# Kernel optimization log

Measured on AMD Instinct MI355X. Metric: run time of the kernel, lower is better.

The kernel has to match this reference:

```python
import jax, jax.numpy as jnp
import numpy as np

B, T, I, H = 512, 256, 256, 512


def _lstm(x, Wih, Whh, bih, bhh):
    # x: [B, T, I]; Wih: [4H, I]; Whh: [4H, H]; gate order i, f, g, o (torch)
    Bv = x.shape[0]
    Hv = Whh.shape[1]
    xg = jnp.einsum('bti,gi->btg', x, Wih) + bih + bhh  # [B, T, 4H] (input projections hoisted out of scan)
    xg = jnp.transpose(xg, (1, 0, 2))  # [T, B, 4H]
    h0 = jnp.zeros((Bv, Hv), x.dtype)
    c0 = jnp.zeros((Bv, Hv), x.dtype)

    def step(carry, gx):
        h, c = carry
        g = gx + h @ Whh.T  # [B, 4H]
        i, f, gg, o = jnp.split(g, 4, axis=-1)
        i = jax.nn.sigmoid(i)
        f = jax.nn.sigmoid(f)
        gg = jnp.tanh(gg)
        o = jax.nn.sigmoid(o)
        c = f * c + i * gg
        h = o * jnp.tanh(c)
        return (h, c), h

    _, hs = jax.lax.scan(step, (h0, c0), xg)  # hs: [T, B, H]
    return jnp.transpose(hs, (1, 0, 2))  # [B, T, H]


def _bn1d(x, gamma, beta, eps=1e-5):
    # torch BatchNorm1d on [N, C, L] in training mode: per-channel stats over (N, L), biased var
    m = jnp.mean(x, axis=(0, 2), keepdims=True)
    v = jnp.var(x, axis=(0, 2), keepdims=True)
    return (x - m) * jax.lax.rsqrt(v + eps) * gamma[None, :, None] + beta[None, :, None]


def setup_inputs() -> dict:
    key = jax.random.key(0)
    ks = jax.random.split(key, 14)
    s = 1.0 / np.sqrt(H)
    return {
        'x': jax.random.normal(ks[0], (B, T, I), jnp.float32),
        'Wih': jax.random.uniform(ks[1], (4 * H, I), jnp.float32, -s, s),
        'Whh': jax.random.uniform(ks[2], (4 * H, H), jnp.float32, -s, s),
        'bih': jax.random.uniform(ks[3], (4 * H,), jnp.float32, -s, s),
        'bhh': jax.random.uniform(ks[4], (4 * H,), jnp.float32, -s, s),
        'fc1_w': jax.random.uniform(ks[5], (32, H), jnp.float32, -s, s),
        'fc1_b': jax.random.uniform(ks[6], (32,), jnp.float32, -s, s),
        'fc2_w': jax.random.uniform(ks[7], (1, 32), jnp.float32, -0.17, 0.17),
        'fc2_b': jax.random.uniform(ks[8], (1,), jnp.float32, -0.17, 0.17),
        'bn1_g': jnp.ones((T,), jnp.float32),
        'bn1_b': jnp.zeros((T,), jnp.float32),
        'bn2_g': jnp.ones((T,), jnp.float32),
        'bn2_b': jnp.zeros((T,), jnp.float32),
    }


def reference(x, Wih, Whh, bih, bhh, fc1_w, fc1_b, fc2_w, fc2_b, bn1_g, bn1_b, bn2_g, bn2_b):
    lstm_out = _lstm(x, Wih, Whh, bih, bhh)  # [B, T, H]
    a = jnp.einsum('bth,oh->bto', lstm_out, fc1_w) + fc1_b  # [B, T, 32]
    a = jax.nn.leaky_relu(_bn1d(a, bn1_g, bn1_b), negative_slope=0.1)
    z = jnp.einsum('bto,po->btp', a, fc2_w) + fc2_b  # [B, T, 1]
    out = jax.nn.relu(_bn1d(z, bn2_g, bn2_b))
    return out
```

## Files before the change

kernel.cpp:

```cpp
#include <hip/hip_runtime.h>

#define BB 512
#define TT 256
#define II 256
#define HH 512

typedef __attribute__((ext_vector_type(8))) short bf16x8;
typedef __attribute__((ext_vector_type(4))) float f32x4;

__device__ __forceinline__ unsigned short f2bf(float f) {
  union { float f; unsigned u; } v; v.f = f;
  unsigned r = v.u + 0x7fffu + ((v.u >> 16) & 1u);
  return (unsigned short)(r >> 16);
}

#define OFF_CNT   0
#define OFF_HSWZ  4096
#define OFF_XSWZ  1052672ULL
#define OFF_HIST  68161536ULL
#define ZERO_WORDS 263168

__global__ void zero_k(unsigned* __restrict__ p, int n) {
  int i = blockIdx.x * blockDim.x + threadIdx.x;
  if (i < n) p[i] = 0u;
}

__global__ __launch_bounds__(256) void prep_x(const float* __restrict__ x,
                                              unsigned char* __restrict__ ws) {
  __shared__ unsigned short xs[16][264];
  const int t = blockIdx.x >> 5, rc = blockIdx.x & 31;
  const int tid = threadIdx.x;
  {
    const int r = tid >> 4, seg = tid & 15;
    const float* src = x + ((size_t)(rc * 16 + r) * TT + t) * II + seg * 16;
    const float4* s4 = (const float4*)src;
#pragma unroll
    for (int q = 0; q < 4; ++q) {
      float4 v = s4[q];
      xs[r][seg * 16 + q * 4 + 0] = f2bf(v.x);
      xs[r][seg * 16 + q * 4 + 1] = f2bf(v.y);
      xs[r][seg * 16 + q * 4 + 2] = f2bf(v.z);
      xs[r][seg * 16 + q * 4 + 3] = f2bf(v.w);
    }
  }
  __syncthreads();
  const int lane = tid & 63;
  const int row16 = lane & 15, koff = (lane >> 4) * 8;
#pragma unroll
  for (int kc = tid >> 6; kc < 8; kc += 4) {
    union { unsigned short h[8]; uint4 v; } pk;
#pragma unroll
    for (int j = 0; j < 8; ++j) pk.h[j] = xs[row16][kc * 32 + koff + j];
    *(uint4*)(ws + OFF_XSWZ + (size_t)(t * 8 + kc) * 32768u +
              ((size_t)rc * 64 + lane) * 16) = pk.v;
  }
}

__global__ __launch_bounds__(512, 2) void lstm_persist(
    const float* __restrict__ Wih, const float* __restrict__ Whh,
    const float* __restrict__ bih, const float* __restrict__ bhh,
    unsigned char* __restrict__ ws)
{
  const int gid = blockIdx.x;
  const int group = gid & 7;
  const int m = gid >> 3;
  const int tid = threadIdx.x;
  const int wv = tid >> 6, lane = tid & 63;
  const int mb = wv & 3, kh = wv >> 2;
  const int lq = lane >> 4, ln = lane & 15;

  int* flags_g = (int*)(ws + OFF_CNT + (size_t)group * 512);
  unsigned char* xswz  = ws + OFF_XSWZ;
  unsigned char* hswz0 = ws + OFF_HSWZ;
  unsigned char* hswz1 = ws + OFF_HSWZ + 524288;
  unsigned char* hist  = ws + OFF_HIST;

  __shared__ int step_flag;
  if (tid == 0) step_flag = 0;

  bf16x8 Wf[12][4];
#pragma unroll
  for (int kk = 0; kk < 12; ++kk) {
    const int kb = (kh * 12 + kk) * 32 + lq * 8;
#pragma unroll
    for (int nt = 0; nt < 4; ++nt) {
      const int gcol = nt * 512 + m * 16 + ln;
      const float* s = (kb < 256) ? (Wih + (size_t)gcol * 256 + kb)
                                  : (Whh + (size_t)gcol * 512 + (kb - 256));
      bf16x8 w;
#pragma unroll
      for (int j = 0; j < 8; ++j) w[j] = (short)f2bf(s[j]);
      Wf[kk][nt] = w;
    }
  }

  float bia[4];
#pragma unroll
  for (int nt = 0; nt < 4; ++nt) {
    int gcol = nt * 512 + m * 16 + ln;
    bia[nt] = bih[gcol] + bhh[gcol];
  }

  __shared__ float g_s[64 * 68];
  __shared__ float h_s[64 * 17];

  const size_t aoff = ((size_t)(group * 4 + mb) * 64 + lane) * 16;
  float creg[4] = {0.f, 0.f, 0.f, 0.f};
  const f32x4 zero4 = {0.f, 0.f, 0.f, 0.f};

#pragma unroll 1
  for (int t = 0; t < 256; ++t) {
    unsigned char* hrd = (t & 1) ? hswz1 : hswz0;
    unsigned char* hwr = (t & 1) ? hswz0 : hswz1;

    f32x4 acc[4] = {zero4, zero4, zero4, zero4};

    if (kh == 0) {
#pragma unroll
      for (int kk = 0; kk < 8; ++kk) {
        bf16x8 a = *(const bf16x8*)(xswz + (size_t)(t * 8 + kk) * 32768u + aoff);
#pragma unroll
        for (int nt = 0; nt < 4; ++nt)
          acc[nt] = __builtin_amdgcn_mfma_f32_16x16x32_bf16(a, Wf[kk][nt], acc[nt], 0, 0, 0);
      }
    }

    if (t > 0) {
      if (kh == 1) {
        int iter = 0;
        for (;;) {
          int v = __hip_atomic_load(flags_g + (lane & 31),
                                    __ATOMIC_RELAXED, __HIP_MEMORY_SCOPE_AGENT);
          if (__all(v >= t)) break;
          if (++iter >= (1 << 17)) break;
          __builtin_amdgcn_s_sleep(1);
        }
        if (wv == 4)
          __hip_atomic_store(&step_flag, t, __ATOMIC_RELAXED,
                             __HIP_MEMORY_SCOPE_WORKGROUP);
      } else {
        int iter = 0;
        while (__hip_atomic_load(&step_flag, __ATOMIC_RELAXED,
                                 __HIP_MEMORY_SCOPE_WORKGROUP) < t
               && iter < (1 << 20)) {
          ++iter;
          __builtin_amdgcn_s_sleep(1);
        }
      }
    }

    if (kh == 0) {
      unsigned long long u0[4], u1[4];
#pragma unroll
      for (int p = 0; p < 4; ++p) {
        const unsigned long long* q =
            (const unsigned long long*)(hrd + (size_t)p * 32768u + aoff);
        u0[p] = __hip_atomic_load(q + 0, __ATOMIC_RELAXED, __HIP_MEMORY_SCOPE_AGENT);
        u1[p] = __hip_atomic_load(q + 1, __ATOMIC_RELAXED, __HIP_MEMORY_SCOPE_AGENT);
      }
#pragma unroll
      for (int kk = 0; kk < 4; ++kk) {
        union { unsigned long long q[2]; bf16x8 v; } u;
        u.q[0] = u0[kk]; u.q[1] = u1[kk];
#pragma unroll
        for (int nt = 0; nt < 4; ++nt)
          acc[nt] = __builtin_amdgcn_mfma_f32_16x16x32_bf16(u.v, Wf[8 + kk][nt], acc[nt], 0, 0, 0);
      }
    } else {
      unsigned long long u0[6], u1[6];
#pragma unroll
      for (int p = 0; p < 6; ++p) {
        const unsigned long long* q =
            (const unsigned long long*)(hrd + (size_t)(4 + p) * 32768u + aoff);
        u0[p] = __hip_atomic_load(q + 0, __ATOMIC_RELAXED, __HIP_MEMORY_SCOPE_AGENT);
        u1[p] = __hip_atomic_load(q + 1, __ATOMIC_RELAXED, __HIP_MEMORY_SCOPE_AGENT);
      }
#pragma unroll
      for (int kk = 0; kk < 12; ++kk) {
        const int slot = kk % 6;
        union { unsigned long long q[2]; bf16x8 v; } u;
        u.q[0] = u0[slot]; u.q[1] = u1[slot];
        if (kk < 6) {
          const unsigned long long* q =
              (const unsigned long long*)(hrd + (size_t)(10 + kk) * 32768u + aoff);
          u0[slot] = __hip_atomic_load(q + 0, __ATOMIC_RELAXED, __HIP_MEMORY_SCOPE_AGENT);
          u1[slot] = __hip_atomic_load(q + 1, __ATOMIC_RELAXED, __HIP_MEMORY_SCOPE_AGENT);
        }
#pragma unroll
        for (int nt = 0; nt < 4; ++nt)
          acc[nt] = __builtin_amdgcn_mfma_f32_16x16x32_bf16(u.v, Wf[kk][nt], acc[nt], 0, 0, 0);
      }
#pragma unroll
      for (int nt = 0; nt < 4; ++nt)
#pragma unroll
        for (int r = 0; r < 4; ++r)
          g_s[(mb * 16 + lq * 4 + r) * 68 + nt * 16 + ln] = acc[nt][r];
    }
    __syncthreads();

    if (kh == 0) {
#pragma unroll
      for (int r = 0; r < 4; ++r) {
        const int rw = mb * 16 + lq * 4 + r;
        float gi = acc[0][r] + g_s[rw * 68 + ln]      + bia[0];
        float gf = acc[1][r] + g_s[rw * 68 + 16 + ln] + bia[1];
        float gg = acc[2][r] + g_s[rw * 68 + 32 + ln] + bia[2];
        float go = acc[3][r] + g_s[rw * 68 + 48 + ln] + bia[3];
        float iv = 1.f / (1.f + __expf(-gi));
        float fv = 1.f / (1.f + __expf(-gf));
        float gv = 1.f - 2.f / (__expf(2.f * gg) + 1.f);
        float ov = 1.f / (1.f + __expf(-go));
        float cv = fv * creg[r] + iv * gv;
        creg[r] = cv;
        h_s[rw * 17 + ln] = ov * (1.f - 2.f / (__expf(2.f * cv) + 1.f));
      }
    }
    __syncthreads();

    if (tid < 256) {
      int rc_l = tid >> 6;
      int rem = tid & 63;
      int lane_off = rem >> 1;
      int half = rem & 1;
      int l2 = (m & 1) * 32 + lane_off;
      int rowl = rc_l * 16 + (lane_off & 15);
      int jb = (lane_off >> 4) * 8 + half * 4;
      union { ushort4 s; unsigned long long q; } pk;
      pk.s = make_ushort4(f2bf(h_s[rowl * 17 + jb + 0]),
                          f2bf(h_s[rowl * 17 + jb + 1]),
                          f2bf(h_s[rowl * 17 + jb + 2]),
                          f2bf(h_s[rowl * 17 + jb + 3]));
      size_t off = ((size_t)((m >> 1) * 32 + group * 4 + rc_l) * 64 + l2) * 16 + half * 8;
      *(unsigned long long*)(hwr + off) = pk.q;
    }
    __syncthreads();

    if (tid == 0)
      __hip_atomic_store(flags_g + m, t + 1, __ATOMIC_RELAXED,
                         __HIP_MEMORY_SCOPE_AGENT);

    if (tid < 256) {
      int row = tid >> 2, jb = (tid & 3) * 4;
      ushort4 hq = make_ushort4(f2bf(h_s[row * 17 + jb + 0]),
                                f2bf(h_s[row * 17 + jb + 1]),
                                f2bf(h_s[row * 17 + jb + 2]),
                                f2bf(h_s[row * 17 + jb + 3]));
      int b = group * 64 + row;
      *(ushort4*)(hist + ((size_t)(b * 256 + t) * 512 + m * 16 + jb) * 2) = hq;
    }
  }
}

__global__ __launch_bounds__(256) void e1_fc1(
    const float* __restrict__ fc1_w, const unsigned char* __restrict__ hist,
    float* __restrict__ a_out)
{
  const int tid = threadIdx.x, wv = tid >> 6, lane = tid & 63;
  const int lq = lane >> 4, ln = lane & 15;

  bf16x8 Bf[16][2];
#pragma unroll
  for (int kk = 0; kk < 16; ++kk) {
#pragma unroll
    for (int nt = 0; nt < 2; ++nt) {
      const float* s = fc1_w + (size_t)(nt * 16 + ln) * 512 + kk * 32 + lq * 8;
      bf16x8 w;
#pragma unroll
      for (int j = 0; j < 8; ++j) w[j] = (short)f2bf(s[j]);
      Bf[kk][nt] = w;
    }
  }

  const int rbase = blockIdx.x * 128 + wv * 32;
  const f32x4 zero4 = {0.f, 0.f, 0.f, 0.f};
  f32x4 acc[2][2] = {{zero4, zero4}, {zero4, zero4}};
#pragma unroll
  for (int kk = 0; kk < 16; ++kk) {
    bf16x8 a0 = *(const bf16x8*)(hist + ((size_t)(rbase + ln) * 512 + kk * 32 + lq * 8) * 2);
    bf16x8 a1 = *(const bf16x8*)(hist + ((size_t)(rbase + 16 + ln) * 512 + kk * 32 + lq * 8) * 2);
#pragma unroll
    for (int nt = 0; nt < 2; ++nt) {
      acc[0][nt] = __builtin_amdgcn_mfma_f32_16x16x32_bf16(a0, Bf[kk][nt], acc[0][nt], 0, 0, 0);
      acc[1][nt] = __builtin_amdgcn_mfma_f32_16x16x32_bf16(a1, Bf[kk][nt], acc[1][nt], 0, 0, 0);
    }
  }
#pragma unroll
  for (int mt = 0; mt < 2; ++mt)
#pragma unroll
    for (int nt = 0; nt < 2; ++nt)
#pragma unroll
      for (int r = 0; r < 4; ++r) {
        int row = rbase + mt * 16 + lq * 4 + r;
        a_out[(size_t)row * 32 + nt * 16 + ln] = acc[mt][nt][r];
      }
}

__global__ __launch_bounds__(256) void e2_head(
    const float* __restrict__ a_in, const float* __restrict__ fc1_b,
    const float* __restrict__ fc2_w, const float* __restrict__ fc2_b,
    const float* __restrict__ bn1_g, const float* __restrict__ bn1_b,
    const float* __restrict__ bn2_g, const float* __restrict__ bn2_b,
    float* __restrict__ out)
{
  const int t = blockIdx.x, tid = threadIdx.x;
  __shared__ float fb[32], fw[32];
  __shared__ float red[4][2], red2[4][2];
  if (tid < 32) { fb[tid] = fc1_b[tid]; fw[tid] = fc2_w[tid]; }
  __syncthreads();

  float va[2][32];
  float s1 = 0.f, s2 = 0.f;
#pragma unroll
  for (int rr = 0; rr < 2; ++rr) {
    int b = tid * 2 + rr;
    const float* p = a_in + ((size_t)b * 256 + t) * 32;
#pragma unroll
    for (int o = 0; o < 32; ++o) {
      float v = p[o] + fb[o];
      va[rr][o] = v;
      s1 += v; s2 += v * v;
    }
  }
#pragma unroll
  for (int off = 32; off > 0; off >>= 1) {
    s1 += __shfl_down(s1, off);
    s2 += __shfl_down(s2, off);
  }
  if ((tid & 63) == 0) { red[tid >> 6][0] = s1; red[tid >> 6][1] = s2; }
  __syncthreads();
  float tot1 = red[0][0] + red[1][0] + red[2][0] + red[3][0];
  float tot2 = red[0][1] + red[1][1] + red[2][1] + red[3][1];
  float m1 = tot1 * (1.f / 16384.f);
  float v1 = tot2 * (1.f / 16384.f) - m1 * m1;
  float sc1 = bn1_g[t] * rsqrtf(v1 + 1e-5f);
  float sh1 = bn1_b[t];

  float z[2];
  float zs1 = 0.f, zs2 = 0.f;
#pragma unroll
  for (int rr = 0; rr < 2; ++rr) {
    float acc = fc2_b[0];
#pragma unroll
    for (int o = 0; o < 32; ++o) {
      float av = (va[rr][o] - m1) * sc1 + sh1;
      av = (av > 0.f) ? av : 0.1f * av;
      acc += av * fw[o];
    }
    z[rr] = acc; zs1 += acc; zs2 += acc * acc;
  }
#pragma unroll
  for (int off = 32; off > 0; off >>= 1) {
    zs1 += __shfl_down(zs1, off);
    zs2 += __shfl_down(zs2, off);
  }
  if ((tid & 63) == 0) { red2[tid >> 6][0] = zs1; red2[tid >> 6][1] = zs2; }
  __syncthreads();
  float zt1 = red2[0][0] + red2[1][0] + red2[2][0] + red2[3][0];
  float zt2 = red2[0][1] + red2[1][1] + red2[2][1] + red2[3][1];
  float m2 = zt1 * (1.f / 512.f);
  float v2 = zt2 * (1.f / 512.f) - m2 * m2;
  float sc2 = bn2_g[t] * rsqrtf(v2 + 1e-5f);
  float sh2 = bn2_b[t];
#pragma unroll
  for (int rr = 0; rr < 2; ++rr) {
    int b = tid * 2 + rr;
    float res = (z[rr] - m2) * sc2 + sh2;
    out[(size_t)b * 256 + t] = (res > 0.f) ? res : 0.f;
  }
}

extern "C" void kernel_launch(void* const* d_in, const int* in_sizes, int n_in,
                              void* d_out, int out_size, void* d_ws, size_t ws_size,
                              hipStream_t stream) {
  const float* x    = (const float*)d_in[0];
  const float* Wih  = (const float*)d_in[1];
  const float* Whh  = (const float*)d_in[2];
  const float* bih  = (const float*)d_in[3];
  const float* bhh  = (const float*)d_in[4];
  const float* fc1w = (const float*)d_in[5];
  const float* fc1b = (const float*)d_in[6];
  const float* fc2w = (const float*)d_in[7];
  const float* fc2b = (const float*)d_in[8];
  const float* b1g  = (const float*)d_in[9];
  const float* b1b  = (const float*)d_in[10];
  const float* b2g  = (const float*)d_in[11];
  const float* b2b  = (const float*)d_in[12];
  unsigned char* ws = (unsigned char*)d_ws;
  float* out = (float*)d_out;
  float* a_buf = (float*)(ws + OFF_XSWZ);

  zero_k<<<1028, 256, 0, stream>>>((unsigned*)ws, ZERO_WORDS);
  prep_x<<<8192, 256, 0, stream>>>(x, ws);
  lstm_persist<<<256, 512, 0, stream>>>(Wih, Whh, bih, bhh, ws);
  e1_fc1<<<1024, 256, 0, stream>>>(fc1w, ws + OFF_HIST, a_buf);
  e2_head<<<256, 256, 0, stream>>>(a_buf, fc1b, fc2w, fc2b, b1g, b1b, b2g, b2b, out);
}
```

Before: 1.552 ms.

## Prefetch next-step x operands and drop a per-step block barrier in LSTM loop

The x-projection operands for step t+1 are now loaded into registers during step t, right after the h loads are issued. This takes global-load latency off the serial recurrence path. The kh==1 waves now issue all twelve h-chunk loads up front instead of using a six-slot rotating buffer. The barrier before the gate math becomes a raw s_barrier with an explicit lgkmcnt wait, and the bf16 packing of h is moved into the same waves that compute it, which removes one __syncthreads per step. This adds register pressure and relies on each wave only reading the h_s rows it wrote itself.

```diff
diff --git a/kernel.cpp b/kernel.cpp
--- a/kernel.cpp
+++ b/kernel.cpp
@@ -108,6 +108,13 @@
   float creg[4] = {0.f, 0.f, 0.f, 0.f};
   const f32x4 zero4 = {0.f, 0.f, 0.f, 0.f};
 
+  bf16x8 xv[8];
+  if (kh == 0) {
+#pragma unroll
+    for (int kk = 0; kk < 8; ++kk)
+      xv[kk] = *(const bf16x8*)(xswz + (size_t)kk * 32768u + aoff);
+  }
+
 #pragma unroll 1
   for (int t = 0; t < 256; ++t) {
     unsigned char* hrd = (t & 1) ? hswz1 : hswz0;
@@ -117,20 +124,18 @@
 
     if (kh == 0) {
 #pragma unroll
-      for (int kk = 0; kk < 8; ++kk) {
-        bf16x8 a = *(const bf16x8*)(xswz + (size_t)(t * 8 + kk) * 32768u + aoff);
+      for (int kk = 0; kk < 8; ++kk)
 #pragma unroll
         for (int nt = 0; nt < 4; ++nt)
-          acc[nt] = __builtin_amdgcn_mfma_f32_16x16x32_bf16(a, Wf[kk][nt], acc[nt], 0, 0, 0);
-      }
+          acc[nt] = __builtin_amdgcn_mfma_f32_16x16x32_bf16(xv[kk], Wf[kk][nt], acc[nt], 0, 0, 0);
     }
 
     if (t > 0) {
       if (kh == 1) {
         int iter = 0;
         for (;;) {
-          int v = __hip_atomic_load(flags_g + (lane & 31),
-                                    __ATOMIC_RELAXED, __HIP_MEMORY_SCOPE_AGENT);
+          int v = __hip_atomic_load(flags_g + (lane & 31), __ATOMIC_RELAXED,
+                                    __HIP_MEMORY_SCOPE_AGENT);
           if (__all(v >= t)) break;
           if (++iter >= (1 << 17)) break;
           __builtin_amdgcn_s_sleep(1);
@@ -147,6 +152,7 @@
           __builtin_amdgcn_s_sleep(1);
         }
       }
+      asm volatile("" ::: "memory");
     }
 
     if (kh == 0) {
@@ -158,6 +164,12 @@
         u0[p] = __hip_atomic_load(q + 0, __ATOMIC_RELAXED, __HIP_MEMORY_SCOPE_AGENT);
         u1[p] = __hip_atomic_load(q + 1, __ATOMIC_RELAXED, __HIP_MEMORY_SCOPE_AGENT);
       }
+      {
+        const int tn = (t + 1) & 255;
+#pragma unroll
+        for (int kk = 0; kk < 8; ++kk)
+          xv[kk] = *(const bf16x8*)(xswz + (size_t)(tn * 8 + kk) * 32768u + aoff);
+      }
 #pragma unroll
       for (int kk = 0; kk < 4; ++kk) {
         union { unsigned long long q[2]; bf16x8 v; } u;
@@ -167,9 +179,9 @@
           acc[nt] = __builtin_amdgcn_mfma_f32_16x16x32_bf16(u.v, Wf[8 + kk][nt], acc[nt], 0, 0, 0);
       }
     } else {
-      unsigned long long u0[6], u1[6];
-#pragma unroll
-      for (int p = 0; p < 6; ++p) {
+      unsigned long long u0[12], u1[12];
+#pragma unroll
+      for (int p = 0; p < 12; ++p) {
         const unsigned long long* q =
             (const unsigned long long*)(hrd + (size_t)(4 + p) * 32768u + aoff);
         u0[p] = __hip_atomic_load(q + 0, __ATOMIC_RELAXED, __HIP_MEMORY_SCOPE_AGENT);
@@ -177,15 +189,8 @@
       }
 #pragma unroll
       for (int kk = 0; kk < 12; ++kk) {
-        const int slot = kk % 6;
         union { unsigned long long q[2]; bf16x8 v; } u;
-        u.q[0] = u0[slot]; u.q[1] = u1[slot];
-        if (kk < 6) {
-          const unsigned long long* q =
-              (const unsigned long long*)(hrd + (size_t)(10 + kk) * 32768u + aoff);
-          u0[slot] = __hip_atomic_load(q + 0, __ATOMIC_RELAXED, __HIP_MEMORY_SCOPE_AGENT);
-          u1[slot] = __hip_atomic_load(q + 1, __ATOMIC_RELAXED, __HIP_MEMORY_SCOPE_AGENT);
-        }
+        u.q[0] = u0[kk]; u.q[1] = u1[kk];
 #pragma unroll
         for (int nt = 0; nt < 4; ++nt)
           acc[nt] = __builtin_amdgcn_mfma_f32_16x16x32_bf16(u.v, Wf[kk][nt], acc[nt], 0, 0, 0);
@@ -196,7 +201,11 @@
         for (int r = 0; r < 4; ++r)
           g_s[(mb * 16 + lq * 4 + r) * 68 + nt * 16 + ln] = acc[nt][r];
     }
-    __syncthreads();
+
+    asm volatile("s_waitcnt lgkmcnt(0)" ::: "memory");
+    __builtin_amdgcn_sched_barrier(0);
+    __builtin_amdgcn_s_barrier();
+    __builtin_amdgcn_sched_barrier(0);
 
     if (kh == 0) {
 #pragma unroll
@@ -214,24 +223,24 @@
         creg[r] = cv;
         h_s[rw * 17 + ln] = ov * (1.f - 2.f / (__expf(2.f * cv) + 1.f));
       }
-    }
-    __syncthreads();
-
-    if (tid < 256) {
-      int rc_l = tid >> 6;
-      int rem = tid & 63;
-      int lane_off = rem >> 1;
-      int half = rem & 1;
-      int l2 = (m & 1) * 32 + lane_off;
-      int rowl = rc_l * 16 + (lane_off & 15);
-      int jb = (lane_off >> 4) * 8 + half * 4;
-      union { ushort4 s; unsigned long long q; } pk;
-      pk.s = make_ushort4(f2bf(h_s[rowl * 17 + jb + 0]),
-                          f2bf(h_s[rowl * 17 + jb + 1]),
-                          f2bf(h_s[rowl * 17 + jb + 2]),
-                          f2bf(h_s[rowl * 17 + jb + 3]));
-      size_t off = ((size_t)((m >> 1) * 32 + group * 4 + rc_l) * 64 + l2) * 16 + half * 8;
-      *(unsigned long long*)(hwr + off) = pk.q;
+      __builtin_amdgcn_sched_barrier(0);
+
+      {
+        int rc_l = tid >> 6;
+        int rem = tid & 63;
+        int lane_off = rem >> 1;
+        int half = rem & 1;
+        int l2 = (m & 1) * 32 + lane_off;
+        int rowl = rc_l * 16 + (lane_off & 15);
+        int jb = (lane_off >> 4) * 8 + half * 4;
+        union { ushort4 s; unsigned long long q; } pk;
+        pk.s = make_ushort4(f2bf(h_s[rowl * 17 + jb + 0]),
+                            f2bf(h_s[rowl * 17 + jb + 1]),
+                            f2bf(h_s[rowl * 17 + jb + 2]),
+                            f2bf(h_s[rowl * 17 + jb + 3]));
+        size_t off = ((size_t)((m >> 1) * 32 + group * 4 + rc_l) * 64 + l2) * 16 + half * 8;
+        *(unsigned long long*)(hwr + off) = pk.q;
+      }
     }
     __syncthreads();
 
```

Measured after the change: 1.899 ms. 22.4% more time.
